# Kernel optimization log

Measured on AMD Instinct MI355X. Metric: run time of the kernel, lower is better.

Reference implementation:

```python
import jax, jax.numpy as jnp
import numpy as np

B, NQ, NK = 16, 2048, 2048
KD, QD, KQ = 256, 256, 256
CLIP = 10.0


def setup_inputs() -> dict:
    key = jax.random.key(0)
    k1, k2, k3, k4, k5 = jax.random.split(key, 5)
    k_inputs = jax.random.normal(k1, (B, NK, KD), dtype=jnp.float32)
    q_inputs = jax.random.normal(k2, (B, NQ, QD), dtype=jnp.float32)
    adjancy = jax.random.randint(k3, (B, NQ, NK), 0, 2, dtype=jnp.int32)
    # Linear init in source: (rand - 0.5) * 0.05 -> uniform(-0.025, 0.025)
    Wk = jax.random.uniform(k4, (KD, KQ), dtype=jnp.float32, minval=-0.025, maxval=0.025)
    Wq = jax.random.uniform(k5, (QD, KQ), dtype=jnp.float32, minval=-0.025, maxval=0.025)
    return {"k_inputs": k_inputs, "q_inputs": q_inputs, "adjancy": adjancy, "Wk": Wk, "Wq": Wq}


def reference(k_inputs, q_inputs, adjancy, Wk, Wq):
    k = jnp.einsum("bnd,de->bne", k_inputs, Wk)          # [B, NK, KQ]
    q = jnp.einsum("bmd,de->bme", q_inputs, Wq)          # [B, NQ, KQ]
    scale = 1.0 / jnp.sqrt(jnp.asarray(KQ, dtype=q.dtype))
    scores = jnp.einsum("bme,bne->bmn", q, k) * scale     # [B, NQ, NK]
    scores = jnp.tanh(scores) * CLIP                      # clip is not None
    scores = jnp.where(adjancy.astype(bool), scores, -jnp.inf)
    return jax.nn.softmax(scores, axis=2)
```

## Files before the change

### kernel.cpp

```cpp
#include <hip/hip_runtime.h>

#define BATCH 16
#define NQ 2048
#define NK 2048

typedef short s16x8 __attribute__((ext_vector_type(8)));
typedef __bf16 bf16x8 __attribute__((ext_vector_type(8)));
typedef float f32x16 __attribute__((ext_vector_type(16)));
typedef float f32x4 __attribute__((ext_vector_type(4)));
typedef unsigned u32x2 __attribute__((ext_vector_type(2)));

static __device__ __forceinline__ unsigned short f2bf(float f) {
  unsigned u = __builtin_bit_cast(unsigned, f);
  u += 0x7FFFu + ((u >> 16) & 1u);
  return (unsigned short)(u >> 16);
}

static __device__ __forceinline__ f32x16 mfma32(s16x8 a, s16x8 b, f32x16 c) {
  return __builtin_amdgcn_mfma_f32_32x32x16_bf16(
      __builtin_bit_cast(bf16x8, a), __builtin_bit_cast(bf16x8, b), c, 0, 0, 0);
}

static __device__ __forceinline__ f32x4 mfma16(s16x8 a, s16x8 b, f32x4 c) {
  return __builtin_amdgcn_mfma_f32_16x16x32_bf16(
      __builtin_bit_cast(bf16x8, a), __builtin_bit_cast(bf16x8, b), c, 0, 0, 0);
}

static __device__ __forceinline__ float score_p(float s) {
  float u = __builtin_amdgcn_exp2f(s * 2.885390081777927f);
  return __builtin_amdgcn_exp2f(-28.853900817779268f * __builtin_amdgcn_rcpf(u + 1.0f));
}

__global__ void prep_wt(const float* __restrict__ Wk, unsigned short* __restrict__ WkT,
                        const float* __restrict__ Wq, unsigned short* __restrict__ WqT) {
  const float* W = blockIdx.y ? Wq : Wk;
  unsigned short* WT = blockIdx.y ? WqT : WkT;
  float scale = blockIdx.y ? 0.0625f : 1.0f;
  int idx = blockIdx.x * 256 + threadIdx.x;
  int n = idx >> 8, k = idx & 255;
  WT[n * 256 + k] = f2bf(W[k * 256 + n] * scale);
}

__global__ __launch_bounds__(256, 2) void proj_kernel(
    const float* __restrict__ Xk, const unsigned short* __restrict__ WkT,
    unsigned short* __restrict__ Yk,
    const float* __restrict__ Xq, const unsigned short* __restrict__ WqT,
    unsigned short* __restrict__ Yq) {
  const float* X;
  const unsigned short* WT;
  unsigned short* Y;
  if (blockIdx.y == 0) { X = Xk; WT = WkT; Y = Yk; }
  else                 { X = Xq; WT = WqT; Y = Yq; }

  int tid = threadIdx.x;
  int wave = tid >> 6, lane = tid & 63;
  int l31 = lane & 31, kh = lane >> 5;
  int r0 = blockIdx.x * 128 + wave * 32;

  const float* xp = X + (size_t)(r0 + l31) * 256 + kh * 8;

  f32x16 acc[8];
#pragma unroll
  for (int ct = 0; ct < 8; ++ct)
#pragma unroll
    for (int i = 0; i < 16; ++i) acc[ct][i] = 0.0f;

#pragma unroll
  for (int kk = 0; kk < 16; ++kk) {
    f32x4 a0 = *(const f32x4*)(xp + kk * 16);
    f32x4 a1 = *(const f32x4*)(xp + kk * 16 + 4);
    s16x8 af;
#pragma unroll
    for (int j = 0; j < 4; ++j) {
      af[j]     = (short)f2bf(a0[j]);
      af[4 + j] = (short)f2bf(a1[j]);
    }
#pragma unroll
    for (int ct = 0; ct < 8; ++ct) {
      s16x8 bw = *(const s16x8*)(WT + (size_t)(ct * 32 + l31) * 256 + kk * 16 + kh * 8);
      acc[ct] = mfma32(af, bw, acc[ct]);
    }
  }

  int kg2 = l31 >> 3, j = l31 & 7;
#pragma unroll
  for (int ct = 0; ct < 8; ++ct) {
#pragma unroll
    for (int r = 0; r < 16; ++r) {
      int rrow = (r & 3) + 8 * (r >> 2) + 4 * kh;
      int row = r0 + rrow;
      Y[((size_t)((row >> 4) * 8 + ct) * 64 + kg2 * 16 + (row & 15)) * 8 + j] =
          f2bf(acc[ct][r]);
    }
  }
}

__global__ __launch_bounds__(512, 2) void attn_kernel(
    const unsigned short* __restrict__ Kf, const unsigned short* __restrict__ Qf,
    const int* __restrict__ adj, float* __restrict__ out) {
  int lin = blockIdx.y * 128 + blockIdx.x;
  int b  = (lin & 7) * 2 + ((lin >> 3) & 1);
  int qt = lin >> 4;
  int q0 = qt * 16;
  int tid = threadIdx.x;
  int wave = tid >> 6, lane = tid & 63;
  int l15 = lane & 15, kg = lane >> 4;
  int colbase = wave * 256;

  __shared__ unsigned plds[8 * 16 * 64 * 2];
  __shared__ unsigned lmask[8 * 144];
  __shared__ float wsum[8][16];
  __shared__ float rrecip[16];

  const unsigned short* qp = Qf + (size_t)(b * 128 + qt) * 8 * 512;
  s16x8 aq[8];
#pragma unroll
  for (int kk = 0; kk < 8; ++kk)
    aq[kk] = *(const s16x8*)(qp + ((size_t)kk * 64 + lane) * 8);

  const int* abase = adj + ((size_t)b * NQ + q0) * (size_t)NK + colbase + lane;
  unsigned* lm = lmask + wave * 144;
#pragma unroll
  for (int r = 0; r < 16; ++r) {
    const int* ap = abase + (size_t)r * NK;
    int a0 = ap[0], a1 = ap[64], a2 = ap[128], a3 = ap[192];
    unsigned long long b0 = __ballot(a0 != 0);
    unsigned long long b1 = __ballot(a1 != 0);
    unsigned long long b2 = __ballot(a2 != 0);
    unsigned long long b3 = __ballot(a3 != 0);
    if (lane < 8) {
      unsigned long long bb = (lane & 4) ? ((lane & 2) ? b3 : b2)
                                         : ((lane & 2) ? b1 : b0);
      unsigned word = (lane & 1) ? (unsigned)(bb >> 32) : (unsigned)bb;
      lm[r * 9 + lane] = word;
    }
  }

  const unsigned short* kfb = Kf + (size_t)b * 128 * 8 * 512;
  unsigned* pl = plds + (wave * 16) * 128 + lane * 2;

  float rsum[4] = {0.0f, 0.0f, 0.0f, 0.0f};

#pragma unroll 2
  for (int ct = 0; ct < 16; ++ct) {
    f32x4 acc = {0.0f, 0.0f, 0.0f, 0.0f};
    const unsigned short* kpt = kfb + (size_t)(wave * 16 + ct) * 8 * 512;
#pragma unroll
    for (int kk = 0; kk < 8; ++kk) {
      s16x8 bk = *(const s16x8*)(kpt + ((size_t)kk * 64 + lane) * 8);
      acc = mfma16(aq[kk], bk, acc);
    }
    unsigned shift = (unsigned)((ct & 1) * 16 + l15);
    float p[4];
#pragma unroll
    for (int r = 0; r < 4; ++r) {
      unsigned mw = lm[(kg * 4 + r) * 9 + (ct >> 1)];
      float e = score_p(acc[r]);
      p[r] = ((mw >> shift) & 1u) ? e : 0.0f;
      rsum[r] += p[r];
    }
    unsigned lo = (unsigned)f2bf(p[0]) | ((unsigned)f2bf(p[1]) << 16);
    unsigned hi = (unsigned)f2bf(p[2]) | ((unsigned)f2bf(p[3]) << 16);
    u32x2 v; v[0] = lo; v[1] = hi;
    *(u32x2*)(pl + ct * 128) = v;
  }

#pragma unroll
  for (int r = 0; r < 4; ++r) {
    float v = rsum[r];
    v += __shfl_xor(v, 1);
    v += __shfl_xor(v, 2);
    v += __shfl_xor(v, 4);
    v += __shfl_xor(v, 8);
    rsum[r] = v;
  }
  if (l15 == 0) {
#pragma unroll
    for (int r = 0; r < 4; ++r) wsum[wave][kg * 4 + r] = rsum[r];
  }
  __syncthreads();
  if (tid < 16) {
    float s = 0.0f;
#pragma unroll
    for (int w = 0; w < 8; ++w) s += wsum[w][tid];
    rrecip[tid] = 1.0f / s;
  }
  __syncthreads();

  float rc[4];
#pragma unroll
  for (int r = 0; r < 4; ++r) rc[r] = rrecip[kg * 4 + r];

  float* op = out + ((size_t)b * NQ + q0 + kg * 4) * (size_t)NK + colbase + l15;
#pragma unroll 4
  for (int ct = 0; ct < 16; ++ct) {
    u32x2 v = *(const u32x2*)(pl + ct * 128);
    float p0 = __builtin_bit_cast(float, v[0] << 16);
    float p1 = __builtin_bit_cast(float, v[0] & 0xffff0000u);
    float p2 = __builtin_bit_cast(float, v[1] << 16);
    float p3 = __builtin_bit_cast(float, v[1] & 0xffff0000u);
    op[(size_t)0 * NK + ct * 16] = p0 * rc[0];
    op[(size_t)1 * NK + ct * 16] = p1 * rc[1];
    op[(size_t)2 * NK + ct * 16] = p2 * rc[2];
    op[(size_t)3 * NK + ct * 16] = p3 * rc[3];
  }
}

extern "C" void kernel_launch(void* const* d_in, const int* in_sizes, int n_in,
                              void* d_out, int out_size, void* d_ws, size_t ws_size,
                              hipStream_t stream) {
  const float* k_in = (const float*)d_in[0];
  const float* q_in = (const float*)d_in[1];
  const int* adj    = (const int*)d_in[2];
  const float* Wk   = (const float*)d_in[3];
  const float* Wq   = (const float*)d_in[4];
  float* out = (float*)d_out;

  char* ws = (char*)d_ws;
  unsigned short* WkT = (unsigned short*)(ws);
  unsigned short* WqT = (unsigned short*)(ws + (1u << 17));
  unsigned short* Kf  = (unsigned short*)(ws + (1u << 18));
  unsigned short* Qf  = (unsigned short*)(ws + (1u << 18) + (1u << 24));

  prep_wt<<<dim3(256, 2), 256, 0, stream>>>(Wk, WkT, Wq, WqT);

  proj_kernel<<<dim3(256, 2), 256, 0, stream>>>(k_in, WkT, Kf, q_in, WqT, Qf);

  attn_kernel<<<dim3(128, 16), 512, 0, stream>>>(Kf, Qf, adj, out);
}
```

Measured before the change: 255.8 us.

## Vectorize adjacency mask loads, keep probabilities in registers, nontemporal output stores

Adjacency rows are now read as 16-byte nontemporal vector loads, eight rows at a time, and packed into bitmasks with lane shuffles instead of scalar loads plus ballots. The bf16 probability staging buffer moves from LDS into fully unrolled per-thread register arrays, and the normalized output is written with nontemporal stores. The aim is fewer memory instructions and less cache pollution on the two large streams (adjacency in, output out), and dropping the LDS round trip. In exchange, register pressure rises from the unrolled loops and register-held arrays, which could reduce occupancy or cause spills.

```diff
diff --git a/kernel.cpp b/kernel.cpp
--- a/kernel.cpp
+++ b/kernel.cpp
@@ -8,7 +8,7 @@
 typedef __bf16 bf16x8 __attribute__((ext_vector_type(8)));
 typedef float f32x16 __attribute__((ext_vector_type(16)));
 typedef float f32x4 __attribute__((ext_vector_type(4)));
-typedef unsigned u32x2 __attribute__((ext_vector_type(2)));
+typedef int i32x4 __attribute__((ext_vector_type(4)));
 
 static __device__ __forceinline__ unsigned short f2bf(float f) {
   unsigned u = __builtin_bit_cast(unsigned, f);
@@ -107,7 +107,6 @@
   int l15 = lane & 15, kg = lane >> 4;
   int colbase = wave * 256;
 
-  __shared__ unsigned plds[8 * 16 * 64 * 2];
   __shared__ unsigned lmask[8 * 144];
   __shared__ float wsum[8][16];
   __shared__ float rrecip[16];
@@ -118,30 +117,34 @@
   for (int kk = 0; kk < 8; ++kk)
     aq[kk] = *(const s16x8*)(qp + ((size_t)kk * 64 + lane) * 8);
 
-  const int* abase = adj + ((size_t)b * NQ + q0) * (size_t)NK + colbase + lane;
+  const i32x4* ap4 =
+      (const i32x4*)(adj + ((size_t)b * NQ + q0) * (size_t)NK + colbase) + lane;
   unsigned* lm = lmask + wave * 144;
 #pragma unroll
-  for (int r = 0; r < 16; ++r) {
-    const int* ap = abase + (size_t)r * NK;
-    int a0 = ap[0], a1 = ap[64], a2 = ap[128], a3 = ap[192];
-    unsigned long long b0 = __ballot(a0 != 0);
-    unsigned long long b1 = __ballot(a1 != 0);
-    unsigned long long b2 = __ballot(a2 != 0);
-    unsigned long long b3 = __ballot(a3 != 0);
-    if (lane < 8) {
-      unsigned long long bb = (lane & 4) ? ((lane & 2) ? b3 : b2)
-                                         : ((lane & 2) ? b1 : b0);
-      unsigned word = (lane & 1) ? (unsigned)(bb >> 32) : (unsigned)bb;
-      lm[r * 9 + lane] = word;
+  for (int half = 0; half < 2; ++half) {
+    i32x4 av[8];
+#pragma unroll
+    for (int r8 = 0; r8 < 8; ++r8)
+      av[r8] = __builtin_nontemporal_load(ap4 + (size_t)(half * 8 + r8) * (NK / 4));
+#pragma unroll
+    for (int r8 = 0; r8 < 8; ++r8) {
+      i32x4 v = av[r8];
+      unsigned nib = (v[0] != 0 ? 1u : 0u) | (v[1] != 0 ? 2u : 0u) |
+                     (v[2] != 0 ? 4u : 0u) | (v[3] != 0 ? 8u : 0u);
+      unsigned m = nib << ((lane & 7) * 4);
+      m |= __shfl_xor(m, 1);
+      m |= __shfl_xor(m, 2);
+      m |= __shfl_xor(m, 4);
+      if ((lane & 7) == 0) lm[(half * 8 + r8) * 9 + (lane >> 3)] = m;
     }
   }
 
   const unsigned short* kfb = Kf + (size_t)b * 128 * 8 * 512;
-  unsigned* pl = plds + (wave * 16) * 128 + lane * 2;
 
   float rsum[4] = {0.0f, 0.0f, 0.0f, 0.0f};
-
-#pragma unroll 2
+  unsigned pstl[16], psth[16];
+
+#pragma unroll
   for (int ct = 0; ct < 16; ++ct) {
     f32x4 acc = {0.0f, 0.0f, 0.0f, 0.0f};
     const unsigned short* kpt = kfb + (size_t)(wave * 16 + ct) * 8 * 512;
@@ -159,10 +162,8 @@
       p[r] = ((mw >> shift) & 1u) ? e : 0.0f;
       rsum[r] += p[r];
     }
-    unsigned lo = (unsigned)f2bf(p[0]) | ((unsigned)f2bf(p[1]) << 16);
-    unsigned hi = (unsigned)f2bf(p[2]) | ((unsigned)f2bf(p[3]) << 16);
-    u32x2 v; v[0] = lo; v[1] = hi;
-    *(u32x2*)(pl + ct * 128) = v;
+    pstl[ct] = (unsigned)f2bf(p[0]) | ((unsigned)f2bf(p[1]) << 16);
+    psth[ct] = (unsigned)f2bf(p[2]) | ((unsigned)f2bf(p[3]) << 16);
   }
 
 #pragma unroll
@@ -192,17 +193,16 @@
   for (int r = 0; r < 4; ++r) rc[r] = rrecip[kg * 4 + r];
 
   float* op = out + ((size_t)b * NQ + q0 + kg * 4) * (size_t)NK + colbase + l15;
-#pragma unroll 4
+#pragma unroll
   for (int ct = 0; ct < 16; ++ct) {
-    u32x2 v = *(const u32x2*)(pl + ct * 128);
-    float p0 = __builtin_bit_cast(float, v[0] << 16);
-    float p1 = __builtin_bit_cast(float, v[0] & 0xffff0000u);
-    float p2 = __builtin_bit_cast(float, v[1] << 16);
-    float p3 = __builtin_bit_cast(float, v[1] & 0xffff0000u);
-    op[(size_t)0 * NK + ct * 16] = p0 * rc[0];
-    op[(size_t)1 * NK + ct * 16] = p1 * rc[1];
-    op[(size_t)2 * NK + ct * 16] = p2 * rc[2];
-    op[(size_t)3 * NK + ct * 16] = p3 * rc[3];
+    float p0 = __builtin_bit_cast(float, pstl[ct] << 16);
+    float p1 = __builtin_bit_cast(float, pstl[ct] & 0xffff0000u);
+    float p2 = __builtin_bit_cast(float, psth[ct] << 16);
+    float p3 = __builtin_bit_cast(float, psth[ct] & 0xffff0000u);
+    __builtin_nontemporal_store(p0 * rc[0], op + (size_t)0 * NK + ct * 16);
+    __builtin_nontemporal_store(p1 * rc[1], op + (size_t)1 * NK + ct * 16);
+    __builtin_nontemporal_store(p2 * rc[2], op + (size_t)2 * NK + ct * 16);
+    __builtin_nontemporal_store(p3 * rc[3], op + (size_t)3 * NK + ct * 16);
   }
 }
 
```

After: 278.7 us. +8.9%, slower.
